# Kernel tuning notes

Measured on AMD Instinct MI355X. Metric: run time of the kernel, lower is better.

## Reference

```python
import jax, jax.numpy as jnp
import numpy as np

B, S, E = 2, 2048, 1024
H, D = 16, 64  # NUM_ATTENTION_HEADS, NUM_FEATURES
LN_EPS = 1e-5


def setup_inputs() -> dict:
    key = jax.random.key(0)
    ks = jax.random.split(key, 10)
    scale = 1.0 / np.sqrt(E)
    return {
        "x": jax.random.normal(ks[0], (B, S, E), dtype=jnp.float32),
        "ln_g": jnp.ones((E,), dtype=jnp.float32),
        "ln_b": jnp.zeros((E,), dtype=jnp.float32),
        "wq": jax.random.normal(ks[1], (E, H * D), dtype=jnp.float32) * scale,
        "bq": jnp.zeros((H * D,), dtype=jnp.float32),
        "wk": jax.random.normal(ks[2], (E, H * D), dtype=jnp.float32) * scale,
        "bk": jnp.zeros((H * D,), dtype=jnp.float32),
        "wv": jax.random.normal(ks[3], (E, H * D), dtype=jnp.float32) * scale,
        "bv": jnp.zeros((H * D,), dtype=jnp.float32),
        "wo": jax.random.normal(ks[4], (H * D, E), dtype=jnp.float32) * scale,
        "bo": jnp.zeros((E,), dtype=jnp.float32),
    }


def reference(x, ln_g, ln_b, wq, bq, wk, bk, wv, bv, wo, bo):
    x_residual = x
    # LayerNorm over last dim
    mean = jnp.mean(x, axis=-1, keepdims=True)
    var = jnp.mean(jnp.square(x - mean), axis=-1, keepdims=True)
    xn = (x - mean) * jax.lax.rsqrt(var + LN_EPS) * ln_g + ln_b

    q = (xn @ wq + bq).reshape(B, S, H, D)
    k = (xn @ wk + bk).reshape(B, S, H, D)
    v = (xn @ wv + bv).reshape(B, S, H, D)

    # scores: [B, S_q, S_k, H]
    score = jnp.einsum('bihd,bjhd->bijh', q, k) / np.sqrt(D).astype(np.float32)
    # causal mask: position i may not attend to j > i
    causal = jnp.tril(jnp.ones((S, S), dtype=bool))  # True = keep
    score = jnp.where(causal[None, :, :, None], score, -jnp.inf)
    probs = jax.nn.softmax(score, axis=2)

    out = jnp.einsum('bijh,bjhd->bihd', probs, v).reshape(B, S, H * D)
    out = out @ wo + bo
    return out + x_residual
```

## Files before the change

### kernel.cpp

```cpp
#include <hip/hip_runtime.h>
#include <math.h>
#include <stdint.h>

typedef short short8 __attribute__((ext_vector_type(8)));
typedef short s16x4 __attribute__((ext_vector_type(4)));
typedef float f32x4 __attribute__((ext_vector_type(4)));

constexpr int BB = 2, SS = 2048, EE = 1024, HH = 16, DD = 64, HD = 1024;
constexpr int NROW = BB * SS;
constexpr size_t WELEM = (size_t)1024 * 1024;
constexpr float LN_EPS = 1e-5f;

__device__ const int ENT_QT[40] = {0,1,2,3, 4,4, 5,5, 6,6, 7,7,
                                   8,8,8, 9,9,9, 10,10,10, 11,11,11,
                                   12,12,12,12, 13,13,13,13, 14,14,14,14, 15,15,15,15};
__device__ const int ENT_C0[40] = {0,0,0,0, 0,1, 0,1, 0,1, 0,1,
                                   0,1,2, 0,1,2, 0,1,2, 0,1,2,
                                   0,1,2,3, 0,1,2,3, 0,1,2,3, 0,1,2,3};
__device__ const int EBASE[16]  = {0,1,2,3,4,6,8,10,12,15,18,21,24,28,32,36};
constexpr int NENT = 40;

#if defined(__has_builtin)
#if __has_builtin(__builtin_amdgcn_exp2f)
#define EXP2F(x) __builtin_amdgcn_exp2f(x)
#endif
#endif
#ifndef EXP2F
#define EXP2F(x) exp2f(x)
#endif

__device__ inline short f2bf(float f) {
    union { float f; uint32_t u; } v; v.f = f;
    uint32_t r = (v.u + 0x7fffu + ((v.u >> 16) & 1u)) >> 16;
    return (short)(uint16_t)r;
}

__device__ inline float bf2f(short s) {
    return __uint_as_float(((uint32_t)(uint16_t)s) << 16);
}

__device__ inline uint32_t pk2bf(float f0, float f1) {
    uint32_t u0 = __float_as_uint(f0) + 0x8000u;
    uint32_t u1 = __float_as_uint(f1) + 0x8000u;
    return __builtin_amdgcn_perm(u1, u0, 0x07060302u);
}

__device__ inline uint32_t pk2bf_t(float f0, float f1) {
    return __builtin_amdgcn_perm(__float_as_uint(f1), __float_as_uint(f0), 0x07060302u);
}

__device__ inline s16x4 pack_bf16x4(f32x4 v) {
    union { uint32_t u[2]; s16x4 s; } r;
    r.u[0] = pk2bf(v[0], v[1]);
    r.u[1] = pk2bf(v[2], v[3]);
    return r.s;
}

#define GLOBAL_TO_LDS16(g, l) \
    __builtin_amdgcn_global_load_lds( \
        (const __attribute__((address_space(1))) void*)(g), \
        (__attribute__((address_space(3))) void*)(l), 16, 0, 0)

__global__ void prep_kernel(const float* __restrict__ x,
                            const float* __restrict__ g,
                            const float* __restrict__ b,
                            short* __restrict__ xn,
                            const float* __restrict__ w0, const float* __restrict__ w1,
                            const float* __restrict__ w2, const float* __restrict__ w3,
                            short* __restrict__ wdst) {
    const int bx = blockIdx.x;
    const int t = threadIdx.x;
    if (bx < NROW) {
        const int row = bx;
        const float* xr = x + (size_t)row * EE;
        short* onr = xn + (size_t)row * EE;
        float4 v = ((const float4*)xr)[t];
        float s  = v.x + v.y + v.z + v.w;
        float ss = v.x * v.x + v.y * v.y + v.z * v.z + v.w * v.w;
        #pragma unroll
        for (int o = 32; o > 0; o >>= 1) {
            s  += __shfl_down(s, o);
            ss += __shfl_down(ss, o);
        }
        __shared__ float sm[4], sm2[4];
        const int wid = t >> 6, lane = t & 63;
        if (lane == 0) { sm[wid] = s; sm2[wid] = ss; }
        __syncthreads();
        float ts  = sm[0] + sm[1] + sm[2] + sm[3];
        float tss = sm2[0] + sm2[1] + sm2[2] + sm2[3];
        float mean = ts * (1.0f / EE);
        float var  = tss * (1.0f / EE) - mean * mean;
        float inv  = rsqrtf(var + LN_EPS);
        float4 gv = ((const float4*)g)[t];
        float4 bv = ((const float4*)b)[t];
        s16x4 st;
        st.x = f2bf((v.x - mean) * inv * gv.x + bv.x);
        st.y = f2bf((v.y - mean) * inv * gv.y + bv.y);
        st.z = f2bf((v.z - mean) * inv * gv.z + bv.z);
        st.w = f2bf((v.w - mean) * inv * gv.w + bv.w);
        ((s16x4*)onr)[t] = st;
    } else {
        const int widx = bx - NROW;
        const int z = widx >> 10;
        const int rem = widx & 1023;
        const int k0 = (rem >> 5) * 32, p0 = (rem & 31) * 32;
        const float* src = (z == 0) ? w0 : (z == 1) ? w1 : (z == 2) ? w2 : w3;
        short* d = wdst + (size_t)z * WELEM;
        __shared__ float tile[32][33];
        const int tx = t & 31, ty = t >> 5;
        #pragma unroll
        for (int r = ty; r < 32; r += 8)
            tile[r][tx] = src[(size_t)(k0 + r) * 1024 + p0 + tx];
        __syncthreads();
        #pragma unroll
        for (int r = ty; r < 32; r += 8)
            d[(size_t)(p0 + r) * 1024 + k0 + tx] = f2bf(tile[tx][r]);
    }
}

template <bool F32OUT>
__global__ __launch_bounds__(256) void mfma_gemm(
    const short* __restrict__ A,
    const short* __restrict__ BtBase,
    const float* __restrict__ b0, const float* __restrict__ b1,
    const float* __restrict__ b2,
    short* __restrict__ outB, short* __restrict__ outV,
    const float* __restrict__ resid, float* __restrict__ outF) {
    constexpr int K = 1024, N = 1024;
    const int t = threadIdx.x, lane = t & 63, w = t >> 6;
    const int quad = lane >> 4, l16 = lane & 15;
    const int wm = w >> 1, wn = w & 1;
    const int row0 = blockIdx.y * 128, col0 = blockIdx.x * 128;
    const int z = blockIdx.z;
    const short* Bt = BtBase + (size_t)z * WELEM;
    const float* bias = (z == 0) ? b0 : (z == 1) ? b1 : b2;

    __shared__ short As[128 * 32];
    __shared__ short Bs[128 * 32];

    f32x4 acc[4][4];
    #pragma unroll
    for (int i = 0; i < 4; i++)
        #pragma unroll
        for (int j = 0; j < 4; j++) acc[i][j] = (f32x4){0.f, 0.f, 0.f, 0.f};

    const int srow = t >> 2, schunk = t & 3;
    const short* agp = A  + (size_t)(row0 + srow) * K + schunk * 8;
    const short* bgp = Bt + (size_t)(col0 + srow) * K + schunk * 8;

    for (int k0 = 0; k0 < K; k0 += 32) {
        GLOBAL_TO_LDS16(agp + k0,                    As + t * 8);
        GLOBAL_TO_LDS16(agp + (size_t)64 * K + k0,   As + 2048 + t * 8);
        GLOBAL_TO_LDS16(bgp + k0,                    Bs + t * 8);
        GLOBAL_TO_LDS16(bgp + (size_t)64 * K + k0,   Bs + 2048 + t * 8);
        __syncthreads();
        short8 af[4], bf[4];
        #pragma unroll
        for (int mt = 0; mt < 4; mt++)
            af[mt] = *(const short8*)&As[(wm * 64 + mt * 16 + l16) * 32 + quad * 8];
        #pragma unroll
        for (int nt = 0; nt < 4; nt++)
            bf[nt] = *(const short8*)&Bs[(wn * 64 + nt * 16 + l16) * 32 + quad * 8];
        #pragma unroll
        for (int mt = 0; mt < 4; mt++)
            #pragma unroll
            for (int nt = 0; nt < 4; nt++)
                acc[mt][nt] = __builtin_amdgcn_mfma_f32_16x16x32_bf16(
                    af[mt], bf[nt], acc[mt][nt], 0, 0, 0);
        __syncthreads();
    }

    #pragma unroll
    for (int mt = 0; mt < 4; mt++) {
        #pragma unroll
        for (int nt = 0; nt < 4; nt++) {
            const int rbase = row0 + wm * 64 + mt * 16 + quad * 4;
            const int col = col0 + wn * 64 + nt * 16 + l16;
            const float bcol = bias[col];
            if (F32OUT) {
                #pragma unroll
                for (int r = 0; r < 4; r++)
                    outF[(size_t)(rbase + r) * N + col] =
                        acc[mt][nt][r] + bcol +
                        resid[(size_t)(rbase + r) * N + col];
            } else if (z == 2) {
                union { uint32_t u[2]; s16x4 s; } pk;
                pk.u[0] = pk2bf(acc[mt][nt][0] + bcol, acc[mt][nt][1] + bcol);
                pk.u[1] = pk2bf(acc[mt][nt][2] + bcol, acc[mt][nt][3] + bcol);
                *(s16x4*)&outV[(size_t)col * NROW + rbase] = pk.s;
            } else {
                #pragma unroll
                for (int r = 0; r < 4; r++)
                    outB[(size_t)z * NROW * N + (size_t)(rbase + r) * N + col] =
                        f2bf(acc[mt][nt][r] + bcol);
            }
        }
    }
}

#define ATTN_ITER(JT, DIAG)                                                     \
    {                                                                           \
        const int jt_ = (JT);                                                   \
        if (jt_ + 1 < jt1) {                                                    \
            const size_t ko = (size_t)(jt_ + 1) * 64 * HD;                      \
            const int vo = (jt_ + 1) * 64;                                      \
            const int ob = (buf ^ 1) * 4096;                                    \
            GLOBAL_TO_LDS16(kb0 + ko, Kb + ob + t * 8);                         \
            GLOBAL_TO_LDS16(kb1 + ko, Kb + ob + (t + 256) * 8);                 \
            GLOBAL_TO_LDS16(vb0 + vo, Vb + ob + t * 8);                         \
            GLOBAL_TO_LDS16(vb1 + vo, Vb + ob + (t + 256) * 8);                 \
        }                                                                       \
        const short* Kc = Kb + buf * 4096;                                      \
        const short* Vc = Vb + buf * 4096;                                      \
        f32x4 s[4][2];                                                          \
        _Pragma("unroll")                                                       \
        for (int mj = 0; mj < 4; mj++)                                          \
            _Pragma("unroll")                                                   \
            for (int nt = 0; nt < 2; nt++) s[mj][nt] = (f32x4){0.f,0.f,0.f,0.f};\
        _Pragma("unroll")                                                       \
        for (int ks = 0; ks < 2; ks++) {                                        \
            const int cq = ((ks * 4 + quad) ^ sw) * 8;                          \
            short8 kf[4];                                                       \
            _Pragma("unroll")                                                   \
            for (int mj = 0; mj < 4; mj++)                                      \
                kf[mj] = *(const short8*)&Kc[(mj * 16 + l16) * 64 + cq];        \
            _Pragma("unroll")                                                   \
            for (int mj = 0; mj < 4; mj++)                                      \
                _Pragma("unroll")                                               \
                for (int nt = 0; nt < 2; nt++)                                  \
                    s[mj][nt] = __builtin_amdgcn_mfma_f32_16x16x32_bf16(        \
                        kf[mj], qreg[nt][ks], s[mj][nt], 0, 0, 0);              \
        }                                                                       \
        const int joff = (jt_ - 2 * qt) * 64;                                   \
        _Pragma("unroll")                                                       \
        for (int mj = 0; mj < 4; mj++) {                                        \
            _Pragma("unroll")                                                   \
            for (int nt = 0; nt < 2; nt++) {                                    \
                const int ir = irel + nt * 16;                                  \
                _Pragma("unroll")                                               \
                for (int r = 0; r < 4; r++) {                                   \
                    float p = EXP2F(s[mj][nt][r] * 0.18033688f);                \
                    if (DIAG) {                                                 \
                        const int jrel = joff + mj * 16 + quad * 4 + r;         \
                        if (jrel > ir) p = 0.f;                                 \
                    }                                                           \
                    s[mj][nt][r] = p;                                           \
                }                                                               \
            }                                                                   \
        }                                                                       \
        _Pragma("unroll")                                                       \
        for (int ks2 = 0; ks2 < 4; ks2++) {                                     \
            s16x4 pf[2];                                                        \
            _Pragma("unroll")                                                   \
            for (int nt = 0; nt < 2; nt++) {                                    \
                union { uint32_t u[2]; s16x4 s4; } r_;                          \
                r_.u[0] = pk2bf_t(s[ks2][nt][0], s[ks2][nt][1]);                \
                r_.u[1] = pk2bf_t(s[ks2][nt][2], s[ks2][nt][3]);                \
                pf[nt] = r_.s4;                                                 \
                Lacc[nt] = __builtin_amdgcn_mfma_f32_16x16x16bf16_1k(           \
                    onesf, pf[nt], Lacc[nt], 0, 0, 0);                          \
            }                                                                   \
            _Pragma("unroll")                                                   \
            for (int mtd = 0; mtd < 4; mtd++) {                                 \
                const int cv = (((ks2 * 2 + (quad >> 1)) ^ sw) * 8) + (quad & 1) * 4;\
                s16x4 vf = *(const s16x4*)&Vc[(mtd * 16 + l16) * 64 + cv];      \
                _Pragma("unroll")                                               \
                for (int nt = 0; nt < 2; nt++)                                  \
                    Ot[mtd][nt] = __builtin_amdgcn_mfma_f32_16x16x16bf16_1k(    \
                        vf, pf[nt], Ot[mtd][nt], 0, 0, 0);                      \
            }                                                                   \
        }                                                                       \
        __syncthreads();                                                        \
        buf ^= 1;                                                               \
    }

__global__ __launch_bounds__(256, 4) void attn_split(
    const short* __restrict__ q, const short* __restrict__ kkk,
    const short* __restrict__ vtp,
    short* __restrict__ OpartB, float* __restrict__ lpart,
    short* __restrict__ attno) {
    const int e = NENT - 1 - (int)blockIdx.x;
    const int h = blockIdx.y, b = blockIdx.z;
    const int qt = ENT_QT[e], c0 = ENT_C0[e];
    const int t = threadIdx.x, lane = t & 63, w = t >> 6;
    const int quad = lane >> 4, l16 = lane & 15;
    const int sw = l16 & 7;
    const int i0 = qt * 128;

    __shared__ short Kb[2 * 64 * 64];
    __shared__ short Vb[2 * 64 * 64];

    short8 qreg[2][2];
    const size_t qoff = ((size_t)(b * SS + i0)) * HD + h * DD;
    const short* qrow = q + qoff + (size_t)(w * 32 + l16) * HD + quad * 8;
    #pragma unroll
    for (int nt = 0; nt < 2; nt++)
        #pragma unroll
        for (int ks = 0; ks < 2; ks++)
            qreg[nt][ks] = *(const short8*)(qrow + nt * 16 * HD + ks * 32);

    const int r0 = t >> 3,         cs0 = t & 7;
    const int r1 = (t + 256) >> 3, cs1 = (t + 256) & 7;
    const short* kb0 = kkk + ((size_t)b * SS) * HD + h * DD + (size_t)r0 * HD + (cs0 ^ (r0 & 7)) * 8;
    const short* kb1 = kkk + ((size_t)b * SS) * HD + h * DD + (size_t)r1 * HD + (cs1 ^ (r1 & 7)) * 8;
    const short* vb0 = vtp + ((size_t)(h * 64 + r0)) * NROW + b * SS + (cs0 ^ (r0 & 7)) * 8;
    const short* vb1 = vtp + ((size_t)(h * 64 + r1)) * NROW + b * SS + (cs1 ^ (r1 & 7)) * 8;

    f32x4 Ot[4][2];
    f32x4 Lacc[2];
    #pragma unroll
    for (int mtd = 0; mtd < 4; mtd++)
        #pragma unroll
        for (int nt = 0; nt < 2; nt++) Ot[mtd][nt] = (f32x4){0.f, 0.f, 0.f, 0.f};
    Lacc[0] = (f32x4){0.f, 0.f, 0.f, 0.f};
    Lacc[1] = (f32x4){0.f, 0.f, 0.f, 0.f};
    s16x4 onesf;
    onesf[0] = onesf[1] = onesf[2] = onesf[3] = (short)0x3F80;

    const int jt0 = c0 * 8;
    const int jt1 = min(jt0 + 8, 2 * qt + 2);
    const int irel = w * 32 + l16;

    {
        const size_t ko = (size_t)jt0 * 64 * HD;
        const int vo = jt0 * 64;
        GLOBAL_TO_LDS16(kb0 + ko, Kb + t * 8);
        GLOBAL_TO_LDS16(kb1 + ko, Kb + (t + 256) * 8);
        GLOBAL_TO_LDS16(vb0 + vo, Vb + t * 8);
        GLOBAL_TO_LDS16(vb1 + vo, Vb + (t + 256) * 8);
    }
    __syncthreads();

    int buf = 0;
    const int dmid   = min(jt1, 2 * qt);
    const int dstart = max(jt0, 2 * qt);
    for (int jt = jt0; jt < dmid; ++jt) ATTN_ITER(jt, false)
    for (int jt = dstart; jt < jt1; ++jt) ATTN_ITER(jt, true)

    if (qt < 4) {
        #pragma unroll
        for (int nt = 0; nt < 2; nt++) {
            const float inv = 1.0f / Lacc[nt][0];
            const int i_abs = i0 + w * 32 + nt * 16 + l16;
            const size_t ob = ((size_t)(b * SS + i_abs)) * HD + h * DD;
            #pragma unroll
            for (int mtd = 0; mtd < 4; mtd++) {
                f32x4 val = Ot[mtd][nt];
                union { uint32_t u[2]; s16x4 s4; } pk;
                pk.u[0] = pk2bf(val[0] * inv, val[1] * inv);
                pk.u[1] = pk2bf(val[2] * inv, val[3] * inv);
                *(s16x4*)&attno[ob + mtd * 16 + quad * 4] = pk.s4;
            }
        }
        return;
    }

    const int slot = (b * HH + h) * NENT + e;
    #pragma unroll
    for (int nt = 0; nt < 2; nt++) {
        const int i_rel = w * 32 + nt * 16 + l16;
        if (quad == 0) lpart[(size_t)slot * 128 + i_rel] = Lacc[nt][0];
        #pragma unroll
        for (int mtd = 0; mtd < 4; mtd++)
            *(s16x4*)&OpartB[(size_t)slot * 8192 + i_rel * 64 + mtd * 16 + quad * 4] =
                pack_bf16x4(Ot[mtd][nt]);
    }
}

__global__ __launch_bounds__(256) void attn_reduce(
    const short* __restrict__ OpartB, const float* __restrict__ lpart,
    short* __restrict__ attno) {
    const int qt = 4 + blockIdx.x, h = blockIdx.y, b = blockIdx.z;
    const int t = threadIdx.x;
    const int nch = (qt >> 2) + 1;
    const int slot0 = (b * HH + h) * NENT + EBASE[qt];
    const int i0 = qt * 128;
    #pragma unroll
    for (int it = 0; it < 8; it++) {
        const int g = t + it * 256;
        const int i = g >> 4, d4 = (g & 15) * 4;
        f32x4 acc = (f32x4){0.f, 0.f, 0.f, 0.f};
        float l = 0.f;
        for (int c = 0; c < nch; c++) {
            s16x4 pv = *(const s16x4*)&OpartB[(size_t)(slot0 + c) * 8192 + i * 64 + d4];
            acc[0] += bf2f(pv[0]);
            acc[1] += bf2f(pv[1]);
            acc[2] += bf2f(pv[2]);
            acc[3] += bf2f(pv[3]);
            l += lpart[(size_t)(slot0 + c) * 128 + i];
        }
        const float inv = 1.0f / l;
        union { uint32_t u[2]; s16x4 s; } pk;
        pk.u[0] = pk2bf(acc[0] * inv, acc[1] * inv);
        pk.u[1] = pk2bf(acc[2] * inv, acc[3] * inv);
        *(s16x4*)&attno[((size_t)(b * SS + i0 + i)) * HD + h * DD + d4] = pk.s;
    }
}

extern "C" void kernel_launch(void* const* d_in, const int* in_sizes, int n_in,
                              void* d_out, int out_size, void* d_ws, size_t ws_size,
                              hipStream_t stream) {
    const float* x    = (const float*)d_in[0];
    const float* ln_g = (const float*)d_in[1];
    const float* ln_b = (const float*)d_in[2];
    const float* wq   = (const float*)d_in[3];
    const float* bq   = (const float*)d_in[4];
    const float* wk   = (const float*)d_in[5];
    const float* bk   = (const float*)d_in[6];
    const float* wv   = (const float*)d_in[7];
    const float* bv   = (const float*)d_in[8];
    const float* wo   = (const float*)d_in[9];
    const float* bo   = (const float*)d_in[10];
    float* out = (float*)d_out;

    const size_t buf = (size_t)NROW * HD;
    short* xn    = (short*)d_ws;
    short* qb    = xn + buf;
    short* vt    = qb + 2 * buf;
    short* attno = vt + buf;
    short* wt    = attno + buf;
    short* OpB   = wt + 4 * WELEM;
    float* lpart = (float*)(OpB + (size_t)BB * HH * NENT * 8192);

    prep_kernel<<<2 * NROW, 256, 0, stream>>>(x, ln_g, ln_b, xn,
                                              wq, wk, wv, wo, wt);

    mfma_gemm<false><<<dim3(8, 32, 3), 256, 0, stream>>>(
        xn, wt, bq, bk, bv, qb, vt, nullptr, nullptr);

    attn_split<<<dim3(NENT, HH, BB), 256, 0, stream>>>(
        qb, qb + buf, vt, OpB, lpart, attno);
    attn_reduce<<<dim3(12, HH, BB), 256, 0, stream>>>(OpB, lpart, attno);

    mfma_gemm<true><<<dim3(8, 32, 1), 256, 0, stream>>>(
        attno, wt + 3 * WELEM, bo, bo, bo, nullptr, nullptr, x, out);
}
```

Before: 206.2 us.

## Retile GEMM to 128x64 blocks with K=64 steps and XOR-swizzled LDS

The bf16 MFMA GEMM moves from 128x128 output tiles with a K-step of 32 to 128x64 tiles with a K-step of 64. Each wave now owns a 32x64 strip. The LDS layout is XOR-swizzled to avoid bank conflicts on the fragment reads, and launch bounds now request 4 blocks per CU. The grid doubles in block count so more CUs are busy on the 4096x1024 GEMMs and there are half as many barriers, at the cost of less reuse of each loaded tile.

```diff
diff --git a/kernel.cpp b/kernel.cpp
--- a/kernel.cpp
+++ b/kernel.cpp
@@ -119,7 +119,7 @@
 }
 
 template <bool F32OUT>
-__global__ __launch_bounds__(256) void mfma_gemm(
+__global__ __launch_bounds__(256, 4) void mfma_gemm(
     const short* __restrict__ A,
     const short* __restrict__ BtBase,
     const float* __restrict__ b0, const float* __restrict__ b1,
@@ -129,53 +129,63 @@
     constexpr int K = 1024, N = 1024;
     const int t = threadIdx.x, lane = t & 63, w = t >> 6;
     const int quad = lane >> 4, l16 = lane & 15;
-    const int wm = w >> 1, wn = w & 1;
-    const int row0 = blockIdx.y * 128, col0 = blockIdx.x * 128;
+    const int row0 = blockIdx.x * 128, col0 = blockIdx.y * 64;
     const int z = blockIdx.z;
     const short* Bt = BtBase + (size_t)z * WELEM;
     const float* bias = (z == 0) ? b0 : (z == 1) ? b1 : b2;
 
-    __shared__ short As[128 * 32];
-    __shared__ short Bs[128 * 32];
-
-    f32x4 acc[4][4];
-    #pragma unroll
-    for (int i = 0; i < 4; i++)
+    __shared__ short As[128 * 64];
+    __shared__ short Bs[64 * 64];
+
+    f32x4 acc[2][4];
+    #pragma unroll
+    for (int i = 0; i < 2; i++)
         #pragma unroll
         for (int j = 0; j < 4; j++) acc[i][j] = (f32x4){0.f, 0.f, 0.f, 0.f};
 
-    const int srow = t >> 2, schunk = t & 3;
-    const short* agp = A  + (size_t)(row0 + srow) * K + schunk * 8;
-    const short* bgp = Bt + (size_t)(col0 + srow) * K + schunk * 8;
-
-    for (int k0 = 0; k0 < K; k0 += 32) {
-        GLOBAL_TO_LDS16(agp + k0,                    As + t * 8);
-        GLOBAL_TO_LDS16(agp + (size_t)64 * K + k0,   As + 2048 + t * 8);
-        GLOBAL_TO_LDS16(bgp + k0,                    Bs + t * 8);
-        GLOBAL_TO_LDS16(bgp + (size_t)64 * K + k0,   Bs + 2048 + t * 8);
+    const int sr = t >> 3, sc = t & 7;
+    const int swc = (sc ^ (sr & 7)) * 8;
+    const short* ap0 = A + (size_t)(row0 + sr) * K + swc;
+    const short* ap1 = ap0 + (size_t)32 * K;
+    const short* ap2 = ap0 + (size_t)64 * K;
+    const short* ap3 = ap0 + (size_t)96 * K;
+    const short* bp0 = Bt + (size_t)(col0 + sr) * K + swc;
+    const short* bp1 = bp0 + (size_t)32 * K;
+
+    for (int k0 = 0; k0 < K; k0 += 64) {
+        GLOBAL_TO_LDS16(ap0 + k0, As + t * 8);
+        GLOBAL_TO_LDS16(ap1 + k0, As + (t + 256) * 8);
+        GLOBAL_TO_LDS16(ap2 + k0, As + (t + 512) * 8);
+        GLOBAL_TO_LDS16(ap3 + k0, As + (t + 768) * 8);
+        GLOBAL_TO_LDS16(bp0 + k0, Bs + t * 8);
+        GLOBAL_TO_LDS16(bp1 + k0, Bs + (t + 256) * 8);
         __syncthreads();
-        short8 af[4], bf[4];
-        #pragma unroll
-        for (int mt = 0; mt < 4; mt++)
-            af[mt] = *(const short8*)&As[(wm * 64 + mt * 16 + l16) * 32 + quad * 8];
-        #pragma unroll
-        for (int nt = 0; nt < 4; nt++)
-            bf[nt] = *(const short8*)&Bs[(wn * 64 + nt * 16 + l16) * 32 + quad * 8];
-        #pragma unroll
-        for (int mt = 0; mt < 4; mt++)
+        #pragma unroll
+        for (int ks = 0; ks < 2; ks++) {
+            const int ca = ((ks * 4 + quad) ^ (l16 & 7)) * 8;
+            short8 af[2], bf[4];
+            #pragma unroll
+            for (int mt = 0; mt < 2; mt++)
+                af[mt] = *(const short8*)&As[(w * 32 + mt * 16 + l16) * 64 + ca];
             #pragma unroll
             for (int nt = 0; nt < 4; nt++)
-                acc[mt][nt] = __builtin_amdgcn_mfma_f32_16x16x32_bf16(
-                    af[mt], bf[nt], acc[mt][nt], 0, 0, 0);
+                bf[nt] = *(const short8*)&Bs[(nt * 16 + l16) * 64 + ca];
+            #pragma unroll
+            for (int mt = 0; mt < 2; mt++)
+                #pragma unroll
+                for (int nt = 0; nt < 4; nt++)
+                    acc[mt][nt] = __builtin_amdgcn_mfma_f32_16x16x32_bf16(
+                        af[mt], bf[nt], acc[mt][nt], 0, 0, 0);
+        }
         __syncthreads();
     }
 
     #pragma unroll
-    for (int mt = 0; mt < 4; mt++) {
+    for (int mt = 0; mt < 2; mt++) {
         #pragma unroll
         for (int nt = 0; nt < 4; nt++) {
-            const int rbase = row0 + wm * 64 + mt * 16 + quad * 4;
-            const int col = col0 + wn * 64 + nt * 16 + l16;
+            const int rbase = row0 + w * 32 + mt * 16 + quad * 4;
+            const int col = col0 + nt * 16 + l16;
             const float bcol = bias[col];
             if (F32OUT) {
                 #pragma unroll
@@ -425,13 +435,13 @@
     prep_kernel<<<2 * NROW, 256, 0, stream>>>(x, ln_g, ln_b, xn,
                                               wq, wk, wv, wo, wt);
 
-    mfma_gemm<false><<<dim3(8, 32, 3), 256, 0, stream>>>(
+    mfma_gemm<false><<<dim3(32, 16, 3), 256, 0, stream>>>(
         xn, wt, bq, bk, bv, qb, vt, nullptr, nullptr);
 
     attn_split<<<dim3(NENT, HH, BB), 256, 0, stream>>>(
         qb, qb + buf, vt, OpB, lpart, attno);
     attn_reduce<<<dim3(12, HH, BB), 256, 0, stream>>>(OpB, lpart, attno);
 
-    mfma_gemm<true><<<dim3(8, 32, 1), 256, 0, stream>>>(
+    mfma_gemm<true><<<dim3(32, 16, 1), 256, 0, stream>>>(
         attno, wt + 3 * WELEM, bo, bo, bo, nullptr, nullptr, x, out);
 }
```

Result: no change. 202.5 us (-1.8%).
